# Kernel optimization log

Hardware: AMD Instinct MI355X
Metric: run time of the kernel (lower is better)

## Reference

```python
import jax, jax.numpy as jnp
import numpy as np

PC_RANGE = np.array([-15.0, -30.0, -2.0, 15.0, 30.0, 2.0], dtype=np.float32)
POST_CENTER_RANGE = jnp.array([-20.0, -35.0, -20.0, -35.0, 20.0, 35.0, 20.0, 35.0], dtype=jnp.float32)
MAX_NUM = 100
NUM_CLASSES = 3


def setup_inputs() -> dict:
    key = jax.random.key(0)
    k1, k2, k3 = jax.random.split(key, 3)
    L, B, Q, C, P = 6, 128, 2000, 3, 20
    return {
        "all_cls_scores": jax.random.normal(k1, (L, B, Q, C), dtype=jnp.float32),
        "all_bbox_preds": jax.random.uniform(k2, (L, B, Q, 4), dtype=jnp.float32),
        "all_pts_preds": jax.random.uniform(k3, (L, B, Q, P, 2), dtype=jnp.float32),
    }


def _decode(cls_scores, bbox_preds, pts_preds):
    # cls_scores [B,Q,C], bbox_preds [B,Q,4] (cx,cy,w,h normalized), pts_preds [B,Q,P,2]
    B = cls_scores.shape[0]
    flat = jax.nn.sigmoid(cls_scores).reshape(B, -1)          # [B, Q*C]
    scores, idx = jax.lax.top_k(flat, MAX_NUM)                # [B, M]
    labels = idx % NUM_CLASSES
    bbox_index = idx // NUM_CLASSES
    bbox_s = jnp.take_along_axis(bbox_preds, bbox_index[:, :, None], axis=1)          # [B,M,4]
    pts_s = jnp.take_along_axis(pts_preds, bbox_index[:, :, None, None], axis=1)      # [B,M,P,2]

    # box_center_to_corner: (cx,cy,w,h) -> (x1,y1,x2,y2)
    cx, cy, w, h = jnp.split(bbox_s, 4, axis=-1)
    corners = jnp.concatenate([cx - 0.5 * w, cy - 0.5 * h, cx + 0.5 * w, cy + 0.5 * h], axis=-1)

    sx = PC_RANGE[3] - PC_RANGE[0]
    sy = PC_RANGE[4] - PC_RANGE[1]
    scale = jnp.array([sx, sy, sx, sy], dtype=jnp.float32)
    offset = jnp.array([PC_RANGE[0], PC_RANGE[1], PC_RANGE[0], PC_RANGE[1]], dtype=jnp.float32)
    boxes = corners * scale + offset                           # [B,M,4]

    pts_d = jnp.stack([pts_s[..., 0] * sx + PC_RANGE[0],
                       pts_s[..., 1] * sy + PC_RANGE[1]], axis=-1)  # [B,M,P,2]

    mask = jnp.all(boxes >= POST_CENTER_RANGE[:4], axis=-1) & \
           jnp.all(boxes <= POST_CENTER_RANGE[4:], axis=-1)    # [B,M]
    return boxes, scores, labels, pts_d, mask


def reference(all_cls_scores, all_bbox_preds, all_pts_preds):
    # Only the last decoder layer is decoded, as in MapTRNMSFreeCoder.decode
    boxes, scores, labels, pts, mask = _decode(
        all_cls_scores[-1], all_bbox_preds[-1], all_pts_preds[-1]
    )
    # Torch filters by boolean mask (ragged); here we pad: zero-out masked-off
    # entries and return the mask so downstream can recover the ragged result.
    boxes = jnp.where(mask[..., None], boxes, 0.0)
    scores = jnp.where(mask, scores, 0.0)
    labels = jnp.where(mask, labels, -1)
    pts = jnp.where(mask[..., None, None], pts, 0.0)
    return boxes, scores, labels, pts, mask
```

## Files before the change

### kernel.cpp

```cpp
#include <hip/hip_runtime.h>
#include <math.h>

#define LAYERS 6
#define BATCH 128
#define NQ 2000
#define NC 3
#define NP 20
#define TOPK 100
#define QC (NQ * NC)
#define NTHREADS 256
#define MAXPER 24
#define REM 112
#define TIE_CAP 256

#define BOXES_OFF 0
#define SCORES_OFF 51200
#define LABELS_OFF 64000
#define PTS_OFF 76800
#define MASK_OFF 588800

template <int SHIFT, int NBITS>
__device__ inline void radix_pass(const unsigned int* __restrict__ rv, int cnt,
                                  unsigned int& prefix, unsigned int& pmask, int& need,
                                  int* hist, int* scanb, int* wtot,
                                  int* sBin, int* sGt,
                                  int tid, int lane, int wid)
{
    constexpr int NB = 1 << NBITS;
    constexpr unsigned int DMASK = (unsigned int)(NB - 1);
    constexpr int BP = NB / NTHREADS;

    #pragma unroll
    for (int j = 0; j < BP; ++j) hist[tid * BP + j] = 0;
    __syncthreads();

    for (int k = 0; k < cnt; ++k) {
        const unsigned int u = rv[k];
        if ((u & pmask) == prefix) atomicAdd(&hist[(u >> SHIFT) & DMASK], 1);
    }
    __syncthreads();

    int v[BP];
    int tot = 0;
    #pragma unroll
    for (int j = BP - 1; j >= 0; --j) { tot += hist[tid * BP + j]; v[j] = tot; }

    int incl = tot;
    #pragma unroll
    for (int off = 1; off < 64; off <<= 1) {
        const int o = __shfl_down(incl, off);
        incl += (lane + off < 64) ? o : 0;
    }
    if (lane == 0) wtot[wid] = incl;
    __syncthreads();

    int higher = 0;
    for (int w = wid + 1; w < 4; ++w) higher += wtot[w];
    const int base = higher + (incl - tot);

    #pragma unroll
    for (int j = 0; j < BP; ++j) scanb[tid * BP + j] = base + v[j];
    __syncthreads();

    #pragma unroll
    for (int j = 0; j < BP; ++j) {
        const int bin = tid * BP + j;
        const int s = base + v[j];
        const int nxt = (bin == NB - 1) ? 0 : scanb[bin + 1];
        if (s >= need && (bin == NB - 1 || nxt < need)) { *sBin = bin; *sGt = nxt; }
    }
    __syncthreads();

    prefix |= ((unsigned int)*sBin) << SHIFT;
    pmask |= DMASK << SHIFT;
    need -= *sGt;
}

__global__ __launch_bounds__(NTHREADS) void maptr_post_kernel(
    const float* __restrict__ cls,
    const float* __restrict__ bbox,
    const float* __restrict__ pts,
    float* __restrict__ out)
{
    const int b = blockIdx.x;
    const int tid = threadIdx.x;
    const int lane = tid & 63;
    const int wid = tid >> 6;

    __shared__ int hist[2048];
    __shared__ int scanb[2048];
    __shared__ int wtot[4];
    __shared__ int sBin, sGt;
    __shared__ unsigned int cand_u[TOPK];
    __shared__ int cand_i[TOPK];
    __shared__ int tie_i[TIE_CAP];
    __shared__ int nCand, nTie;
    __shared__ float topv[TOPK];
    __shared__ int topi[TOPK];
    __shared__ int sbi[TOPK];
    __shared__ float smask[TOPK];

    if (tid == 0) { nCand = 0; nTie = 0; }

    const float* clsb = cls + (size_t)b * QC;
    const int cnt = (tid < REM) ? MAXPER : (MAXPER - 1);
    unsigned int rv[MAXPER];
    for (int k = 0; k < cnt; ++k) {
        const unsigned int bits = __float_as_uint(clsb[tid + k * NTHREADS]);
        rv[k] = (bits & 0x80000000u) ? ~bits : (bits | 0x80000000u);
    }

    unsigned int prefix = 0, pmask = 0;
    int need = TOPK;
    radix_pass<21, 11>(rv, cnt, prefix, pmask, need, hist, scanb, wtot, &sBin, &sGt, tid, lane, wid);
    radix_pass<10, 11>(rv, cnt, prefix, pmask, need, hist, scanb, wtot, &sBin, &sGt, tid, lane, wid);
    radix_pass<0, 10>(rv, cnt, prefix, pmask, need, hist, scanb, wtot, &sBin, &sGt, tid, lane, wid);

    const unsigned int T32 = prefix;
    const int R = need;

    for (int k = 0; k < cnt; ++k) {
        const unsigned int u = rv[k];
        const int i = tid + k * NTHREADS;
        if (u > T32) {
            const int p = atomicAdd(&nCand, 1);
            cand_u[p] = u; cand_i[p] = i;
        } else if (u == T32) {
            const int p = atomicAdd(&nTie, 1);
            if (p < TIE_CAP) tie_i[p] = i;
        }
    }
    __syncthreads();
    const int G = nCand;
    const int E = (nTie < TIE_CAP) ? nTie : TIE_CAP;
    if (tid < E) {
        const int mine = tie_i[tid];
        int rk = 0;
        for (int j = 0; j < E; ++j) rk += (tie_i[j] < mine);
        if (rk < R) { cand_u[G + rk] = T32; cand_i[G + rk] = mine; }
    }
    __syncthreads();

    if (tid < TOPK) {
        const unsigned int u = cand_u[tid];
        const int ii = cand_i[tid];
        int rank = 0;
        for (int j = 0; j < TOPK; ++j) {
            const unsigned int uj = cand_u[j];
            const int ij = cand_i[j];
            rank += (uj > u) || (uj == u && ij < ii);
        }
        const unsigned int bits = (u & 0x80000000u) ? (u & 0x7fffffffu) : ~u;
        topv[rank] = __uint_as_float(bits);
        topi[rank] = ii;
    }
    __syncthreads();

    float* const boxes_out = out + BOXES_OFF;
    float* const scores_out = out + SCORES_OFF;
    float* const labels_out = out + LABELS_OFF;
    float* const pts_out = out + PTS_OFF;
    float* const mask_out = out + MASK_OFF;

    if (tid < TOPK) {
        const int m = tid;
        const int idx = topi[m];
        const float lv = topv[m];
        const float score = 1.0f / (1.0f + expf(-lv));
        const int bi = idx / 3;
        const int label = idx - bi * 3;

        const float4 bb = *(const float4*)(bbox + ((size_t)b * NQ + bi) * 4);
        const float bx1 = (bb.x - 0.5f * bb.z) * 30.0f - 15.0f;
        const float by1 = (bb.y - 0.5f * bb.w) * 60.0f - 30.0f;
        const float bx2 = (bb.x + 0.5f * bb.z) * 30.0f - 15.0f;
        const float by2 = (bb.y + 0.5f * bb.w) * 60.0f - 30.0f;

        const bool mk = (bx1 >= -20.0f) && (by1 >= -35.0f) && (bx2 >= -20.0f) && (by2 >= -35.0f) &&
                        (bx1 <= 20.0f) && (by1 <= 35.0f) && (bx2 <= 20.0f) && (by2 <= 35.0f);

        const size_t bm = (size_t)b * TOPK + m;
        boxes_out[bm * 4 + 0] = mk ? bx1 : 0.0f;
        boxes_out[bm * 4 + 1] = mk ? by1 : 0.0f;
        boxes_out[bm * 4 + 2] = mk ? bx2 : 0.0f;
        boxes_out[bm * 4 + 3] = mk ? by2 : 0.0f;
        scores_out[bm] = mk ? score : 0.0f;
        labels_out[bm] = mk ? (float)label : -1.0f;
        mask_out[bm] = mk ? 1.0f : 0.0f;
        sbi[m] = bi;
        smask[m] = mk ? 1.0f : 0.0f;
    }
    __syncthreads();

    for (int t = tid; t < TOPK * NP; t += NTHREADS) {
        const int m = t / NP;
        const int p = t - m * NP;
        const int bi = sbi[m];
        const bool mk = smask[m] != 0.0f;
        const float2 pv = *(const float2*)(pts + (((size_t)b * NQ + bi) * NP + p) * 2);
        const size_t o = (((size_t)b * TOPK + m) * NP + p) * 2;
        pts_out[o + 0] = mk ? (pv.x * 30.0f - 15.0f) : 0.0f;
        pts_out[o + 1] = mk ? (pv.y * 60.0f - 30.0f) : 0.0f;
    }
}

extern "C" void kernel_launch(void* const* d_in, const int* in_sizes, int n_in,
                              void* d_out, int out_size, void* d_ws, size_t ws_size,
                              hipStream_t stream) {
    const float* cls = (const float*)d_in[0] + (size_t)(LAYERS - 1) * BATCH * NQ * NC;
    const float* bbox = (const float*)d_in[1] + (size_t)(LAYERS - 1) * BATCH * NQ * 4;
    const float* pts = (const float*)d_in[2] + (size_t)(LAYERS - 1) * BATCH * NQ * NP * 2;
    maptr_post_kernel<<<BATCH, NTHREADS, 0, stream>>>(cls, bbox, pts, (float*)d_out);
}
```

Before: 317.8 us.

## Replace three-pass radix select with single 11-bit pass plus rank-sort of candidates

The exact 32-bit radix select, which took three histogram passes and a tie-handling step, is replaced with one histogram over the top 11 key bits. Every element whose top bin is at or above the threshold bin becomes a candidate, and candidates are ranked by an all-pairs comparison to pick the top 100. This removes two histogram/scan passes and their barriers, but the candidate set can grow to hundreds of entries, so the O(C^2) rank loop may cost more. Correctness depends on the candidate count staying under the 2048 cap. Padded out-of-range keys are set to 0, and the load loop is fully unrolled.

```diff
diff --git a/kernel.cpp b/kernel.cpp
--- a/kernel.cpp
+++ b/kernel.cpp
@@ -7,74 +7,18 @@
 #define NC 3
 #define NP 20
 #define TOPK 100
-#define QC (NQ * NC)
+#define QC 6000
 #define NTHREADS 256
-#define MAXPER 24
-#define REM 112
-#define TIE_CAP 256
+#define KPT 24
+#define NB 2048
+#define BP (NB / NTHREADS)
+#define CAP 2048
 
 #define BOXES_OFF 0
 #define SCORES_OFF 51200
 #define LABELS_OFF 64000
 #define PTS_OFF 76800
 #define MASK_OFF 588800
-
-template <int SHIFT, int NBITS>
-__device__ inline void radix_pass(const unsigned int* __restrict__ rv, int cnt,
-                                  unsigned int& prefix, unsigned int& pmask, int& need,
-                                  int* hist, int* scanb, int* wtot,
-                                  int* sBin, int* sGt,
-                                  int tid, int lane, int wid)
-{
-    constexpr int NB = 1 << NBITS;
-    constexpr unsigned int DMASK = (unsigned int)(NB - 1);
-    constexpr int BP = NB / NTHREADS;
-
-    #pragma unroll
-    for (int j = 0; j < BP; ++j) hist[tid * BP + j] = 0;
-    __syncthreads();
-
-    for (int k = 0; k < cnt; ++k) {
-        const unsigned int u = rv[k];
-        if ((u & pmask) == prefix) atomicAdd(&hist[(u >> SHIFT) & DMASK], 1);
-    }
-    __syncthreads();
-
-    int v[BP];
-    int tot = 0;
-    #pragma unroll
-    for (int j = BP - 1; j >= 0; --j) { tot += hist[tid * BP + j]; v[j] = tot; }
-
-    int incl = tot;
-    #pragma unroll
-    for (int off = 1; off < 64; off <<= 1) {
-        const int o = __shfl_down(incl, off);
-        incl += (lane + off < 64) ? o : 0;
-    }
-    if (lane == 0) wtot[wid] = incl;
-    __syncthreads();
-
-    int higher = 0;
-    for (int w = wid + 1; w < 4; ++w) higher += wtot[w];
-    const int base = higher + (incl - tot);
-
-    #pragma unroll
-    for (int j = 0; j < BP; ++j) scanb[tid * BP + j] = base + v[j];
-    __syncthreads();
-
-    #pragma unroll
-    for (int j = 0; j < BP; ++j) {
-        const int bin = tid * BP + j;
-        const int s = base + v[j];
-        const int nxt = (bin == NB - 1) ? 0 : scanb[bin + 1];
-        if (s >= need && (bin == NB - 1 || nxt < need)) { *sBin = bin; *sGt = nxt; }
-    }
-    __syncthreads();
-
-    prefix |= ((unsigned int)*sBin) << SHIFT;
-    pmask |= DMASK << SHIFT;
-    need -= *sGt;
-}
 
 __global__ __launch_bounds__(NTHREADS) void maptr_post_kernel(
     const float* __restrict__ cls,
@@ -87,72 +31,94 @@
     const int lane = tid & 63;
     const int wid = tid >> 6;
 
-    __shared__ int hist[2048];
-    __shared__ int scanb[2048];
+    __shared__ int hist[NB];
+    __shared__ int scanb[NB];
     __shared__ int wtot[4];
-    __shared__ int sBin, sGt;
-    __shared__ unsigned int cand_u[TOPK];
-    __shared__ int cand_i[TOPK];
-    __shared__ int tie_i[TIE_CAP];
-    __shared__ int nCand, nTie;
+    __shared__ int sBin;
+    __shared__ unsigned int cand_u[CAP];
+    __shared__ int cand_i[CAP];
+    __shared__ int nCand;
     __shared__ float topv[TOPK];
     __shared__ int topi[TOPK];
     __shared__ int sbi[TOPK];
     __shared__ float smask[TOPK];
 
-    if (tid == 0) { nCand = 0; nTie = 0; }
+    #pragma unroll
+    for (int j = 0; j < BP; ++j) hist[tid * BP + j] = 0;
+    if (tid == 0) nCand = 0;
 
     const float* clsb = cls + (size_t)b * QC;
-    const int cnt = (tid < REM) ? MAXPER : (MAXPER - 1);
-    unsigned int rv[MAXPER];
-    for (int k = 0; k < cnt; ++k) {
-        const unsigned int bits = __float_as_uint(clsb[tid + k * NTHREADS]);
-        rv[k] = (bits & 0x80000000u) ? ~bits : (bits | 0x80000000u);
+    unsigned int rv[KPT];
+    #pragma unroll
+    for (int k = 0; k < KPT; ++k) {
+        const int i = tid + k * NTHREADS;
+        unsigned int key = 0u;
+        if (i < QC) {
+            const unsigned int bits = __float_as_uint(clsb[i]);
+            key = (bits & 0x80000000u) ? ~bits : (bits | 0x80000000u);
+        }
+        rv[k] = key;
     }
+    __syncthreads();
 
-    unsigned int prefix = 0, pmask = 0;
-    int need = TOPK;
-    radix_pass<21, 11>(rv, cnt, prefix, pmask, need, hist, scanb, wtot, &sBin, &sGt, tid, lane, wid);
-    radix_pass<10, 11>(rv, cnt, prefix, pmask, need, hist, scanb, wtot, &sBin, &sGt, tid, lane, wid);
-    radix_pass<0, 10>(rv, cnt, prefix, pmask, need, hist, scanb, wtot, &sBin, &sGt, tid, lane, wid);
+    #pragma unroll
+    for (int k = 0; k < KPT; ++k) atomicAdd(&hist[rv[k] >> 21], 1);
+    __syncthreads();
 
-    const unsigned int T32 = prefix;
-    const int R = need;
+    int v[BP];
+    int tot = 0;
+    #pragma unroll
+    for (int j = BP - 1; j >= 0; --j) { tot += hist[tid * BP + j]; v[j] = tot; }
+    int incl = tot;
+    #pragma unroll
+    for (int off = 1; off < 64; off <<= 1) {
+        const int o = __shfl_down(incl, off);
+        incl += (lane + off < 64) ? o : 0;
+    }
+    if (lane == 0) wtot[wid] = incl;
+    __syncthreads();
+    int higher = 0;
+    #pragma unroll
+    for (int w = 0; w < 4; ++w) higher += (w > wid) ? wtot[w] : 0;
+    const int base = higher + (incl - tot);
+    #pragma unroll
+    for (int j = 0; j < BP; ++j) scanb[tid * BP + j] = base + v[j];
+    __syncthreads();
 
-    for (int k = 0; k < cnt; ++k) {
-        const unsigned int u = rv[k];
-        const int i = tid + k * NTHREADS;
-        if (u > T32) {
+    #pragma unroll
+    for (int j = 0; j < BP; ++j) {
+        const int bin = tid * BP + j;
+        const int s = base + v[j];
+        const int nxt = (bin == NB - 1) ? 0 : scanb[bin + 1];
+        if (s >= TOPK && (bin == NB - 1 || nxt < TOPK)) sBin = bin;
+    }
+    __syncthreads();
+    const unsigned int T = (unsigned int)sBin;
+
+    #pragma unroll
+    for (int k = 0; k < KPT; ++k) {
+        if ((rv[k] >> 21) >= T) {
             const int p = atomicAdd(&nCand, 1);
-            cand_u[p] = u; cand_i[p] = i;
-        } else if (u == T32) {
-            const int p = atomicAdd(&nTie, 1);
-            if (p < TIE_CAP) tie_i[p] = i;
+            if (p < CAP) { cand_u[p] = rv[k]; cand_i[p] = tid + k * NTHREADS; }
         }
     }
     __syncthreads();
-    const int G = nCand;
-    const int E = (nTie < TIE_CAP) ? nTie : TIE_CAP;
-    if (tid < E) {
-        const int mine = tie_i[tid];
-        int rk = 0;
-        for (int j = 0; j < E; ++j) rk += (tie_i[j] < mine);
-        if (rk < R) { cand_u[G + rk] = T32; cand_i[G + rk] = mine; }
-    }
-    __syncthreads();
+    const int C = (nCand < CAP) ? nCand : CAP;
 
-    if (tid < TOPK) {
-        const unsigned int u = cand_u[tid];
-        const int ii = cand_i[tid];
+    for (int s = tid; s < C; s += NTHREADS) {
+        const unsigned int u = cand_u[s];
+        const int ii = cand_i[s];
         int rank = 0;
-        for (int j = 0; j < TOPK; ++j) {
+        for (int j = 0; j < C; ++j) {
             const unsigned int uj = cand_u[j];
             const int ij = cand_i[j];
             rank += (uj > u) || (uj == u && ij < ii);
         }
-        const unsigned int bits = (u & 0x80000000u) ? (u & 0x7fffffffu) : ~u;
-        topv[rank] = __uint_as_float(bits);
-        topi[rank] = ii;
+        if (rank < TOPK) {
+            const unsigned int bits = (u & 0x80000000u) ? (u & 0x7fffffffu) : ~u;
+            topv[rank] = __uint_as_float(bits);
+            topi[rank] = ii;
+        }
     }
     __syncthreads();
 
```

New measurement: 300.8 us. 5.3% less time.
